# Performance work log

Measured on AMD Instinct MI355X. Metric: run time of the kernel, lower is better.

Reference implementation:

```python
import jax, jax.numpy as jnp
import numpy as np

NEG_INF = -1e30  # stand-in for float('-inf') that stays nan-free under softmax


def setup_inputs() -> dict:
    key = jax.random.key(0)
    k0, k1, k2, k3 = jax.random.split(key, 4)
    B, T, E, H = 4, 2048, 1024, 64
    X = jax.random.normal(k0, (B, T, E), dtype=jnp.float32)
    Wq = jax.random.normal(k1, (E, H), dtype=jnp.float32) * (E ** -0.5)
    Wk = jax.random.normal(k2, (E, H), dtype=jnp.float32) * (E ** -0.5)
    Wv = jax.random.normal(k3, (E, H), dtype=jnp.float32) * (E ** -0.5)
    return {"X": X, "Wq": Wq, "Wk": Wk, "Wv": Wv}


def reference(X, Wq, Wk, Wv):
    # X: [B, T, E]; W*: [E, H]
    B, T, C = X.shape
    Q = jnp.einsum('bte,eh->bth', X, Wq)
    K = jnp.einsum('bte,eh->bth', X, Wk)
    V = jnp.einsum('bte,eh->bth', X, Wv)
    # NOTE: original scales by emb_size**-0.5 (C), not head_size**-0.5
    wei = jnp.einsum('bqh,bkh->bqk', Q, K) * (C ** -0.5)  # [B, T, T]
    causal = jnp.tril(jnp.ones((T, T), dtype=bool))
    wei = jnp.where(causal, wei, NEG_INF)
    wei = jax.nn.softmax(wei, axis=-1)
    # dropout rate = 0.0 (eval-mode equivalent) -> identity
    out = jnp.einsum('bqk,bkh->bqh', wei, V)  # [B, T, H]
    return out
```

## Files before the change

### kernel.cpp

```cpp
#include <hip/hip_runtime.h>
#include <hip/hip_bf16.h>

constexpr int Bc = 4;
constexpr int Tc = 2048;
constexpr int Ec = 1024;
constexpr int Hc = 64;
constexpr float SCALE = 0.03125f;

typedef short  short8  __attribute__((ext_vector_type(8)));
typedef float  floatx4 __attribute__((ext_vector_type(4)));

__device__ __forceinline__ unsigned short f2bf(float f) {
    union { float f; unsigned int i; } x;
    x.f = f;
    unsigned int r = x.i + 0x7fffu + ((x.i >> 16) & 1u);
    return (unsigned short)(r >> 16);
}

__global__ __launch_bounds__(256) void prep_w(
    const float* __restrict__ Wq, const float* __restrict__ Wk,
    const float* __restrict__ Wv, unsigned short* __restrict__ Wt)
{
    const float* W = blockIdx.y == 0 ? Wq : (blockIdx.y == 1 ? Wk : Wv);
    unsigned short* D = Wt + (size_t)blockIdx.y * (Ec * Hc);
    const int i0 = blockIdx.x * 1024 + threadIdx.x * 4;
    const float4 f = *(const float4*)(W + i0);
    const float v[4] = {f.x, f.y, f.z, f.w};
    #pragma unroll
    for (int j = 0; j < 4; ++j) {
        const int i = i0 + j;
        D[(i & 63) * Ec + (i >> 6)] = f2bf(v[j]);
    }
}

__global__ __launch_bounds__(256) void qkv_mfma8(
    const float* __restrict__ X, const unsigned short* __restrict__ Wt,
    unsigned short* __restrict__ Q, unsigned short* __restrict__ K,
    unsigned short* __restrict__ Vt)
{
    __shared__ __align__(16) unsigned short Xs[16][136];
    __shared__ __align__(16) unsigned short Ws[3][64][136];

    const int tid  = threadIdx.x;
    const int wv   = tid >> 6;
    const int lane = tid & 63;
    const int quad = lane >> 4;
    const int l16  = lane & 15;
    const size_t row0 = (size_t)blockIdx.x * 16;

    floatx4 acc[3];
    #pragma unroll
    for (int j = 0; j < 3; ++j)
        #pragma unroll
        for (int r = 0; r < 4; ++r) acc[j][r] = 0.f;

    const int xrow = tid >> 4;
    const int xc4  = (tid & 15) * 4;

    for (int k0 = 0; k0 < Ec; k0 += 128) {
        __syncthreads();
        #pragma unroll
        for (int h = 0; h < 2; ++h) {
            const float4 f = *(const float4*)(X + (row0 + xrow) * Ec + k0 + h * 64 + xc4);
            uint2 p;
            p.x = (unsigned int)f2bf(f.x) | ((unsigned int)f2bf(f.y) << 16);
            p.y = (unsigned int)f2bf(f.z) | ((unsigned int)f2bf(f.w) << 16);
            *(uint2*)&Xs[xrow][h * 64 + xc4] = p;
        }
        #pragma unroll
        for (int j = 0; j < 12; ++j) {
            const int flat  = tid + 256 * j;
            const int which = flat >> 10;
            const int r     = (flat >> 4) & 63;
            const int c8    = (flat & 15) * 8;
            *(uint4*)&Ws[which][r][c8] =
                *(const uint4*)(Wt + which * 65536 + r * 1024 + k0 + c8);
        }
        __syncthreads();

        #pragma unroll
        for (int ks = 0; ks < 4; ++ks) {
            const short8 a = *(const short8*)&Xs[l16][ks * 32 + quad * 8];
            short8 b[3];
            #pragma unroll
            for (int j = 0; j < 3; ++j) {
                const int f = 3 * wv + j;
                b[j] = *(const short8*)&Ws[f >> 2][16 * (f & 3) + l16][ks * 32 + quad * 8];
            }
            #pragma unroll
            for (int j = 0; j < 3; ++j)
                acc[j] = __builtin_amdgcn_mfma_f32_16x16x32_bf16(a, b[j], acc[j], 0, 0, 0);
        }
    }

    #pragma unroll
    for (int j = 0; j < 3; ++j) {
        const int f  = 3 * wv + j;
        const int mf = f >> 2, nf = f & 3;
        if (mf < 2) {
            unsigned short* O = mf == 0 ? Q : K;
            #pragma unroll
            for (int r = 0; r < 4; ++r) {
                float x = acc[j][r];
                if (!(x > -1.0e4f && x < 1.0e4f)) x = 11111.0f;
                O[(row0 + quad * 4 + r) * Hc + 16 * nf + l16] = f2bf(x);
            }
        } else {
            const size_t b  = row0 >> 11;
            const int    t0 = (int)(row0 & 2047) + quad * 4;
            unsigned short* VtB = Vt + b * ((size_t)Hc * Tc);
            unsigned int pk[2];
            #pragma unroll
            for (int half = 0; half < 2; ++half) {
                float x0 = acc[j][half * 2 + 0], x1 = acc[j][half * 2 + 1];
                if (!(x0 > -1.0e4f && x0 < 1.0e4f)) x0 = 11111.0f;
                if (!(x1 > -1.0e4f && x1 < 1.0e4f)) x1 = 11111.0f;
                pk[half] = (unsigned int)f2bf(x0) | ((unsigned int)f2bf(x1) << 16);
            }
            uint2 st; st.x = pk[0]; st.y = pk[1];
            *(uint2*)(VtB + (size_t)(16 * nf + l16) * Tc + t0) = st;
        }
    }
}

__global__ __launch_bounds__(512, 4) void attn_mfma5(
    const unsigned short* __restrict__ Q, const unsigned short* __restrict__ K,
    const unsigned short* __restrict__ Vt, float* __restrict__ Out)
{
    __shared__ __align__(16) unsigned short Pb[8][16][72];
    __shared__ __align__(16) float accS[8][16][64];
    __shared__ __align__(16) float lS[8][16][16];

    const int tid  = threadIdx.x;
    const int wv   = tid >> 6;
    const int lane = tid & 63;
    const int quad = lane >> 4;
    const int l16  = lane & 15;
    const int qt   = 127 - blockIdx.x;
    const int b    = blockIdx.y;
    const int qend = qt * 16 + 16;
    const size_t base = (size_t)b * Tc * Hc;
    const unsigned short* VtB = Vt + (size_t)b * Hc * Tc;

    short8 aQ[2];
    #pragma unroll
    for (int ks = 0; ks < 2; ++ks)
        aQ[ks] = *(const short8*)(Q + base +
            (size_t)(qt * 16 + l16) * Hc + ks * 32 + quad * 8);

    floatx4 acc[4];
    float l_st[4];
    #pragma unroll
    for (int nh = 0; nh < 4; ++nh)
        #pragma unroll
        for (int r = 0; r < 4; ++r) acc[nh][r] = 0.f;
    #pragma unroll
    for (int r = 0; r < 4; ++r) l_st[r] = 0.f;

    for (int kb = wv * 64; kb < qend; kb += 512) {
        floatx4 s[4];
        #pragma unroll
        for (int ni = 0; ni < 4; ++ni)
            #pragma unroll
            for (int r = 0; r < 4; ++r) s[ni][r] = 0.f;
        #pragma unroll
        for (int ks = 0; ks < 2; ++ks) {
            short8 bk[4];
            #pragma unroll
            for (int ni = 0; ni < 4; ++ni)
                bk[ni] = *(const short8*)(K + base +
                    (size_t)(kb + 16 * ni + l16) * Hc + ks * 32 + quad * 8);
            #pragma unroll
            for (int ni = 0; ni < 4; ++ni)
                s[ni] = __builtin_amdgcn_mfma_f32_16x16x32_bf16(aQ[ks], bk[ni], s[ni], 0, 0, 0);
        }

        #pragma unroll
        for (int r = 0; r < 4; ++r) {
            const int qrow = qt * 16 + quad * 4 + r;
            #pragma unroll
            for (int ni = 0; ni < 4; ++ni) {
                const int kcol = kb + 16 * ni + l16;
                const float p = (kcol > qrow) ? 0.f : __expf(s[ni][r] * SCALE);
                s[ni][r] = p;
                l_st[r] += p;
            }
        }
        #pragma unroll
        for (int ni = 0; ni < 4; ++ni)
            #pragma unroll
            for (int r = 0; r < 4; ++r)
                Pb[wv][quad * 4 + r][16 * ni + l16] = f2bf(s[ni][r]);

        #pragma unroll
        for (int ks = 0; ks < 2; ++ks) {
            const short8 aP = *(const short8*)&Pb[wv][l16][ks * 32 + quad * 8];
            short8 bv[4];
            #pragma unroll
            for (int nh = 0; nh < 4; ++nh)
                bv[nh] = *(const short8*)(VtB +
                    (size_t)(16 * nh + l16) * Tc + kb + ks * 32 + quad * 8);
            #pragma unroll
            for (int nh = 0; nh < 4; ++nh)
                acc[nh] = __builtin_amdgcn_mfma_f32_16x16x32_bf16(aP, bv[nh], acc[nh], 0, 0, 0);
        }
    }

    #pragma unroll
    for (int nh = 0; nh < 4; ++nh)
        #pragma unroll
        for (int r = 0; r < 4; ++r)
            accS[wv][quad * 4 + r][16 * nh + l16] = acc[nh][r];
    #pragma unroll
    for (int r = 0; r < 4; ++r)
        lS[wv][quad * 4 + r][l16] = l_st[r];
    __syncthreads();

    {
        const int q  = tid >> 5;
        const int h0 = (tid & 31) * 2;
        float denom = 0.f;
        #pragma unroll
        for (int w = 0; w < 8; ++w)
            #pragma unroll
            for (int j = 0; j < 16; ++j)
                denom += lS[w][q][j];
        const float inv = 1.f / denom;
        float2 st;
        float* sp = &st.x;
        #pragma unroll
        for (int c = 0; c < 2; ++c) {
            float o = 0.f;
            #pragma unroll
            for (int w = 0; w < 8; ++w)
                o += accS[w][q][h0 + c];
            o *= inv;
            if (!(o > -1.0e5f && o < 1.0e5f)) o = 555.0f;
            sp[c] = o;
        }
        *(float2*)(Out + base + (size_t)(qt * 16 + q) * Hc + h0) = st;
    }
}

extern "C" void kernel_launch(void* const* d_in, const int* in_sizes, int n_in,
                              void* d_out, int out_size, void* d_ws, size_t ws_size,
                              hipStream_t stream)
{
    const float* X  = (const float*)d_in[0];
    const float* Wq = (const float*)d_in[1];
    const float* Wk = (const float*)d_in[2];
    const float* Wv = (const float*)d_in[3];

    const size_t N = (size_t)Bc * Tc * Hc;
    unsigned short* Wt  = (unsigned short*)d_ws;
    unsigned short* Qws = Wt + 3 * (size_t)Ec * Hc;
    unsigned short* Kws = Qws + N;
    unsigned short* Vtw = Kws + N;

    prep_w<<<dim3(64, 3), dim3(256), 0, stream>>>(Wq, Wk, Wv, Wt);
    qkv_mfma8<<<dim3(512), dim3(256), 0, stream>>>(X, Wt, Qws, Kws, Vtw);
    attn_mfma5<<<dim3(128, 4), dim3(512), 0, stream>>>(
        Qws, Kws, Vtw, (float*)d_out);
}
```

Before: 119.8 us.

## Prefetch QKV tiles into registers, double rows per block, reorder attention blocks

The projection kernel now handles 32 rows per 512-thread block, so each weight tile staged in shared memory is reused by twice as many rows. It also loads the next K-slice of X and W into registers while the current slice is being computed, hiding global-load latency. The attention kernel interleaves batches and query tiles in its block ordering to balance causal work, raises wave priority around MFMA groups, and reduces row sums with warp shuffles instead of a large shared array. The costs are higher register pressure and fewer projection blocks.

```diff
diff --git a/kernel.cpp b/kernel.cpp
--- a/kernel.cpp
+++ b/kernel.cpp
@@ -33,12 +33,12 @@
     }
 }
 
-__global__ __launch_bounds__(256) void qkv_mfma8(
+__global__ __launch_bounds__(512, 2) void qkv_mfma9(
     const float* __restrict__ X, const unsigned short* __restrict__ Wt,
     unsigned short* __restrict__ Q, unsigned short* __restrict__ K,
     unsigned short* __restrict__ Vt)
 {
-    __shared__ __align__(16) unsigned short Xs[16][136];
+    __shared__ __align__(16) unsigned short Xs[32][136];
     __shared__ __align__(16) unsigned short Ws[3][64][136];
 
     const int tid  = threadIdx.x;
@@ -46,7 +46,9 @@
     const int lane = tid & 63;
     const int quad = lane >> 4;
     const int l16  = lane & 15;
-    const size_t row0 = (size_t)blockIdx.x * 16;
+    const int rowh = wv >> 2;
+    const int wq   = wv & 3;
+    const size_t row0 = (size_t)blockIdx.x * 32;
 
     floatx4 acc[3];
     #pragma unroll
@@ -57,34 +59,51 @@
     const int xrow = tid >> 4;
     const int xc4  = (tid & 15) * 4;
 
+    float4 xreg[2];
+    uint4  wreg[6];
+    #pragma unroll
+    for (int h = 0; h < 2; ++h)
+        xreg[h] = *(const float4*)(X + (row0 + xrow) * Ec + h * 64 + xc4);
+    #pragma unroll
+    for (int j = 0; j < 6; ++j) {
+        const int flat = tid + 512 * j;
+        wreg[j] = *(const uint4*)(Wt + (flat >> 10) * 65536 +
+                                  ((flat >> 4) & 63) * 1024 + (flat & 15) * 8);
+    }
+
     for (int k0 = 0; k0 < Ec; k0 += 128) {
         __syncthreads();
         #pragma unroll
         for (int h = 0; h < 2; ++h) {
-            const float4 f = *(const float4*)(X + (row0 + xrow) * Ec + k0 + h * 64 + xc4);
             uint2 p;
-            p.x = (unsigned int)f2bf(f.x) | ((unsigned int)f2bf(f.y) << 16);
-            p.y = (unsigned int)f2bf(f.z) | ((unsigned int)f2bf(f.w) << 16);
+            p.x = (unsigned int)f2bf(xreg[h].x) | ((unsigned int)f2bf(xreg[h].y) << 16);
+            p.y = (unsigned int)f2bf(xreg[h].z) | ((unsigned int)f2bf(xreg[h].w) << 16);
             *(uint2*)&Xs[xrow][h * 64 + xc4] = p;
         }
         #pragma unroll
-        for (int j = 0; j < 12; ++j) {
-            const int flat  = tid + 256 * j;
-            const int which = flat >> 10;
-            const int r     = (flat >> 4) & 63;
-            const int c8    = (flat & 15) * 8;
-            *(uint4*)&Ws[which][r][c8] =
-                *(const uint4*)(Wt + which * 65536 + r * 1024 + k0 + c8);
+        for (int j = 0; j < 6; ++j) {
+            const int flat = tid + 512 * j;
+            *(uint4*)&Ws[flat >> 10][(flat >> 4) & 63][(flat & 15) * 8] = wreg[j];
+        }
+        if (k0 + 128 < Ec) {
+            #pragma unroll
+            for (int h = 0; h < 2; ++h)
+                xreg[h] = *(const float4*)(X + (row0 + xrow) * Ec + (k0 + 128) + h * 64 + xc4);
+            #pragma unroll
+            for (int j = 0; j < 6; ++j) {
+                const int flat = tid + 512 * j;
+                wreg[j] = *(const uint4*)(Wt + (flat >> 10) * 65536 +
+                                          ((flat >> 4) & 63) * 1024 + (k0 + 128) + (flat & 15) * 8);
+            }
         }
         __syncthreads();
-
         #pragma unroll
         for (int ks = 0; ks < 4; ++ks) {
-            const short8 a = *(const short8*)&Xs[l16][ks * 32 + quad * 8];
+            const short8 a = *(const short8*)&Xs[rowh * 16 + l16][ks * 32 + quad * 8];
             short8 b[3];
             #pragma unroll
             for (int j = 0; j < 3; ++j) {
-                const int f = 3 * wv + j;
+                const int f = 3 * wq + j;
                 b[j] = *(const short8*)&Ws[f >> 2][16 * (f & 3) + l16][ks * 32 + quad * 8];
             }
             #pragma unroll
@@ -93,9 +112,10 @@
         }
     }
 
+    const size_t rbase = row0 + rowh * 16;
     #pragma unroll
     for (int j = 0; j < 3; ++j) {
-        const int f  = 3 * wv + j;
+        const int f  = 3 * wq + j;
         const int mf = f >> 2, nf = f & 3;
         if (mf < 2) {
             unsigned short* O = mf == 0 ? Q : K;
@@ -103,11 +123,11 @@
             for (int r = 0; r < 4; ++r) {
                 float x = acc[j][r];
                 if (!(x > -1.0e4f && x < 1.0e4f)) x = 11111.0f;
-                O[(row0 + quad * 4 + r) * Hc + 16 * nf + l16] = f2bf(x);
+                O[(rbase + quad * 4 + r) * Hc + 16 * nf + l16] = f2bf(x);
             }
         } else {
-            const size_t b  = row0 >> 11;
-            const int    t0 = (int)(row0 & 2047) + quad * 4;
+            const size_t b  = rbase >> 11;
+            const int    t0 = (int)(rbase & 2047) + quad * 4;
             unsigned short* VtB = Vt + b * ((size_t)Hc * Tc);
             unsigned int pk[2];
             #pragma unroll
@@ -123,21 +143,23 @@
     }
 }
 
-__global__ __launch_bounds__(512, 4) void attn_mfma5(
+__global__ __launch_bounds__(512, 4) void attn_mfma6(
     const unsigned short* __restrict__ Q, const unsigned short* __restrict__ K,
     const unsigned short* __restrict__ Vt, float* __restrict__ Out)
 {
     __shared__ __align__(16) unsigned short Pb[8][16][72];
     __shared__ __align__(16) float accS[8][16][64];
-    __shared__ __align__(16) float lS[8][16][16];
+    __shared__ __align__(16) float lSr[8][16];
 
     const int tid  = threadIdx.x;
     const int wv   = tid >> 6;
     const int lane = tid & 63;
     const int quad = lane >> 4;
     const int l16  = lane & 15;
-    const int qt   = 127 - blockIdx.x;
-    const int b    = blockIdx.y;
+    const int id   = blockIdx.x + 128 * blockIdx.y;
+    const int jj   = id & 255;
+    const int qt   = (id < 256) ? (127 - (jj >> 2)) : (jj >> 2);
+    const int b    = jj & 3;
     const int qend = qt * 16 + 16;
     const size_t base = (size_t)b * Tc * Hc;
     const unsigned short* VtB = Vt + (size_t)b * Hc * Tc;
@@ -170,9 +192,11 @@
             for (int ni = 0; ni < 4; ++ni)
                 bk[ni] = *(const short8*)(K + base +
                     (size_t)(kb + 16 * ni + l16) * Hc + ks * 32 + quad * 8);
+            __builtin_amdgcn_s_setprio(1);
             #pragma unroll
             for (int ni = 0; ni < 4; ++ni)
                 s[ni] = __builtin_amdgcn_mfma_f32_16x16x32_bf16(aQ[ks], bk[ni], s[ni], 0, 0, 0);
+            __builtin_amdgcn_s_setprio(0);
         }
 
         #pragma unroll
@@ -200,9 +224,11 @@
             for (int nh = 0; nh < 4; ++nh)
                 bv[nh] = *(const short8*)(VtB +
                     (size_t)(16 * nh + l16) * Tc + kb + ks * 32 + quad * 8);
+            __builtin_amdgcn_s_setprio(1);
             #pragma unroll
             for (int nh = 0; nh < 4; ++nh)
                 acc[nh] = __builtin_amdgcn_mfma_f32_16x16x32_bf16(aP, bv[nh], acc[nh], 0, 0, 0);
+            __builtin_amdgcn_s_setprio(0);
         }
     }
 
@@ -212,8 +238,18 @@
         for (int r = 0; r < 4; ++r)
             accS[wv][quad * 4 + r][16 * nh + l16] = acc[nh][r];
     #pragma unroll
-    for (int r = 0; r < 4; ++r)
-        lS[wv][quad * 4 + r][l16] = l_st[r];
+    for (int r = 0; r < 4; ++r) {
+        float v = l_st[r];
+        v += __shfl_xor(v, 1);
+        v += __shfl_xor(v, 2);
+        v += __shfl_xor(v, 4);
+        v += __shfl_xor(v, 8);
+        l_st[r] = v;
+    }
+    if (l16 == 0)
+        #pragma unroll
+        for (int r = 0; r < 4; ++r)
+            lSr[wv][quad * 4 + r] = l_st[r];
     __syncthreads();
 
     {
@@ -222,22 +258,18 @@
         float denom = 0.f;
         #pragma unroll
         for (int w = 0; w < 8; ++w)
-            #pragma unroll
-            for (int j = 0; j < 16; ++j)
-                denom += lS[w][q][j];
+            denom += lSr[w][q];
         const float inv = 1.f / denom;
-        float2 st;
-        float* sp = &st.x;
-        #pragma unroll
-        for (int c = 0; c < 2; ++c) {
-            float o = 0.f;
-            #pragma unroll
-            for (int w = 0; w < 8; ++w)
-                o += accS[w][q][h0 + c];
-            o *= inv;
-            if (!(o > -1.0e5f && o < 1.0e5f)) o = 555.0f;
-            sp[c] = o;
-        }
+        float o0 = 0.f, o1 = 0.f;
+        #pragma unroll
+        for (int w = 0; w < 8; ++w) {
+            const float2 v = *(const float2*)&accS[w][q][h0];
+            o0 += v.x; o1 += v.y;
+        }
+        o0 *= inv; o1 *= inv;
+        if (!(o0 > -1.0e5f && o0 < 1.0e5f)) o0 = 555.0f;
+        if (!(o1 > -1.0e5f && o1 < 1.0e5f)) o1 = 555.0f;
+        float2 st; st.x = o0; st.y = o1;
         *(float2*)(Out + base + (size_t)(qt * 16 + q) * Hc + h0) = st;
     }
 }
@@ -258,7 +290,7 @@
     unsigned short* Vtw = Kws + N;
 
     prep_w<<<dim3(64, 3), dim3(256), 0, stream>>>(Wq, Wk, Wv, Wt);
-    qkv_mfma8<<<dim3(512), dim3(256), 0, stream>>>(X, Wt, Qws, Kws, Vtw);
-    attn_mfma5<<<dim3(128, 4), dim3(512), 0, stream>>>(
+    qkv_mfma9<<<dim3(256), dim3(512), 0, stream>>>(X, Wt, Qws, Kws, Vtw);
+    attn_mfma6<<<dim3(128, 4), dim3(512), 0, stream>>>(
         Qws, Kws, Vtw, (float*)d_out);
 }
```

Result: slower. 130.1 us (+8.6%).
